# Kernel optimization log

Measured on AMD Instinct MI355X. Metric: run time of the kernel, lower is better.

## Reference

```python
import jax, jax.numpy as jnp
import numpy as np

CLIP = 100000.0

def heaviside(x):
    # smooth Heaviside approximation
    return (jnp.tanh(5.0 * x) + 1.0) / 2.0

def snowbucket(s0, t, ddf, tmax):
    ddf = ddf * 5.0
    tmax = tmax * 3.0
    return heaviside(t - tmax) * heaviside(s0) * jnp.minimum(s0, ddf * (t - tmax))

def soilbucket(s1, pet, f, smax, qmax, k):
    k = k / 10.0
    f = f / 10.0
    smax = smax * 1500.0
    qmax = qmax * 50.0
    h_pos = heaviside(s1)
    h_over = heaviside(s1 - smax)
    h_under = heaviside(smax - s1)
    et = h_pos * h_over * pet + h_pos * h_under * pet * (s1 / smax)
    qsub = h_pos * h_over * qmax + h_pos * h_under * qmax * jnp.exp(-f * (smax - s1))
    qsurf = h_pos * h_over * (s1 - smax)
    qst = qsub * k
    qgr = qsub * (1.0 - k)
    return et, qsurf, qst, qgr

def setup_inputs() -> dict:
    key = jax.random.key(0)
    ks = jax.random.split(key, 8)
    B, T = 8192, 1024
    prcp = jax.random.uniform(ks[0], (B, T, 1), jnp.float32) * 10.0   # mm/day
    tmean = jax.random.uniform(ks[1], (B, T, 1), jnp.float32) * 30.0 - 5.0  # deg C
    dayl = jax.random.uniform(ks[2], (B, T, 1), jnp.float32) * 0.5 + 0.25   # day fraction
    inputs = jnp.concatenate([prcp, tmean, dayl], axis=-1)
    def p(i):
        return jax.random.uniform(ks[i], (1,), jnp.float32) * 0.6 + 0.2
    return {"inputs": inputs, "f": p(3), "smax": p(4), "qmax": p(5),
            "ddf": p(6), "tmin": p(7), "tmax": p(3), "k": p(4)}

def reference(inputs, f, smax, qmax, ddf, tmin, tmax, k):
    # inputs: (B, T, 3) = [prcp, tmean, dayl]
    prcp = inputs[:, :, 0]
    tmean = inputs[:, :, 1]
    dayl = inputs[:, :, 2]
    pet = 29.8 * (dayl * 24.0) * 0.611 * jnp.exp(17.3 * tmean / (tmean + 237.3)) / (tmean + 273.2)

    tmin_s = tmin * -3.0

    # scan over time: carry = (s0, s1) each (B,)
    xs = jnp.stack([prcp, tmean, pet], axis=-1).transpose(1, 0, 2)  # (T, B, 3)

    def step(carry, x):
        s0, s1 = carry
        p_, t_, pet_ = x[:, 0], x[:, 1], x[:, 2]
        psnow = heaviside(tmin_s - t_) * p_
        prain = heaviside(t_ - tmin_s) * p_
        m = snowbucket(s0, t_, ddf, tmax)
        et, qsurf, qst, qgr = soilbucket(s1, pet_, f, smax, qmax, k)
        ds0 = psnow - m
        ds1 = prain + m - et - qsurf - qst - qgr
        ns0 = s0 + jnp.clip(ds0, -CLIP, CLIP)
        ns1 = s1 + jnp.clip(ds1, -CLIP, CLIP)
        return (ns0, ns1), (ns0, ns1)

    B = inputs.shape[0]
    init = (jnp.zeros((B,), inputs.dtype), jnp.zeros((B,), inputs.dtype))
    _, (s0_seq, s1_seq) = jax.lax.scan(step, init, xs)
    s0_seq = s0_seq.T  # (B, T)
    s1_seq = s1_seq.T

    # post-hoc flux computation on state sequences (as in call())
    _m = snowbucket(s0_seq, tmean, ddf, tmax)
    et, qsurf, qst, qgr = soilbucket(s1_seq, pet, f, smax, qmax, k)
    # mode == 'normal': note original names qsurf 'qsub' and outputs qsub+qst
    return jnp.stack([qsurf + qst, qgr], axis=-1)  # (B, T, 2)
```

## Files before the change

### kernel.cpp

```cpp
#include <hip/hip_runtime.h>

#define CLIPV 100000.0f
typedef __attribute__((address_space(3))) void as3void;
typedef __attribute__((address_space(1))) void as1void;

__device__ __forceinline__ float fexp2(float x){ return __builtin_amdgcn_exp2f(x); }
__device__ __forceinline__ float frcp(float x){ return __builtin_amdgcn_rcpf(x); }

#define WAIT_VM(N) { asm volatile("s_waitcnt vmcnt(" #N ")" ::: "memory"); \
                     __builtin_amdgcn_sched_barrier(0); }
#define LGKM0_BAR() { asm volatile("s_waitcnt lgkmcnt(0)" ::: "memory"); \
                      __builtin_amdgcn_s_barrier(); }

extern "C" __global__ void __launch_bounds__(128, 1)
prnn_kernel(const float* __restrict__ inp,
            const float* __restrict__ fpar,  const float* __restrict__ smaxp,
            const float* __restrict__ qmaxp, const float* __restrict__ ddfp,
            const float* __restrict__ tminp, const float* __restrict__ tmaxp,
            const float* __restrict__ kp,
            float* __restrict__ out)
{
    __shared__ alignas(16) unsigned char lin[2][13312];
    __shared__ alignas(16) float prodb[2][64 * 84];
    __shared__ alignas(16) float lcons[2][64 * 36];

    const int tid = threadIdx.x;
    const int l   = tid & 63;
    const int wv  = tid >> 6;
    const int c0  = blockIdx.x * 64;

    const float NL = -14.426950408889634f;
    float f10    = fpar[0] * 0.1f;
    float smax_s = smaxp[0] * 1500.0f;
    float qmax_s = qmaxp[0] * 50.0f;
    float ddf5   = ddfp[0] * 5.0f;
    float tmin_s = tminp[0] * -3.0f;
    float tmax3  = tmaxp[0] * 3.0f;
    float k10    = kp[0] * 0.1f;
    float ism    = 1.0f / smax_s;
    float cw     = 14.426950408889634f * tmin_s;
    float Kc     = fexp2(14.426950408889634f * (tmax3 - tmin_s));
    float cf     = 1.4426950408889634f * f10;
    float k1m    = 1.0f - k10;

    const float* gin  = inp + (size_t)c0 * 3072;
    float*       gout = out + (size_t)c0 * 2048;

    if (wv == 1) {
        auto stage_load = [&](int s, int pb) {
            const float* gb = gin + s * 48;
            #pragma unroll
            for (int k2 = 0; k2 < 13; ++k2) {
                unsigned e = (unsigned)(k2 * 64 + l);
                unsigned r = (e * 161321u) >> 21;
                int q = (int)(e - r * 13u);
                q = (q > 11) ? 11 : q;
                const float* g = gb + r * 3072 + q * 4;
                __builtin_amdgcn_global_load_lds((as1void*)g,
                    (as3void*)(&lin[pb][k2 * 1024]), 16, 0, 0);
            }
        };

        auto prod_one = [&](float p, float tm, float dl,
                            float& pr, float& ps, float& pe, float& eg, float& tg) {
            float t1 = tm + 237.3f, t2 = tm + 273.2f;
            float r12 = frcp(t1 * t2);
            float e1  = fexp2(24.958624207f * tm * (r12 * t2));
            pe = 436.9872f * dl * e1 * (r12 * t1);
            float ew = fexp2(fmaf(NL, tm, cw));
            float w  = frcp(1.0f + ew);
            pr = w * p;
            ps = p - pr;
            eg = 1.0f + fminf(ew * Kc, 1e30f);
            tg = ddf5 * (tm - tmax3);
        };

        auto prod_compute = [&](int s) {
            const unsigned char* myrow = &lin[s & 1][l * 208];
            float* o = prodb[s & 1] + l * 84;
            #pragma unroll
            for (int u4 = 0; u4 < 4; ++u4) {
                float4 A = *(const float4*)(myrow + u4 * 48);
                float4 B = *(const float4*)(myrow + u4 * 48 + 16);
                float4 C = *(const float4*)(myrow + u4 * 48 + 32);
                float pr[4], ps[4], pe[4], eg[4], tg[4];
                prod_one(A.x, A.y, A.z, pr[0], ps[0], pe[0], eg[0], tg[0]);
                prod_one(A.w, B.x, B.y, pr[1], ps[1], pe[1], eg[1], tg[1]);
                prod_one(B.z, B.w, C.x, pr[2], ps[2], pe[2], eg[2], tg[2]);
                prod_one(C.y, C.z, C.w, pr[3], ps[3], pe[3], eg[3], tg[3]);
                *(float4*)(o +      u4 * 4) = make_float4(pr[0], pr[1], pr[2], pr[3]);
                *(float4*)(o + 16 + u4 * 4) = make_float4(ps[0], ps[1], ps[2], ps[3]);
                *(float4*)(o + 32 + u4 * 4) = make_float4(pe[0], pe[1], pe[2], pe[3]);
                *(float4*)(o + 48 + u4 * 4) = make_float4(eg[0], eg[1], eg[2], eg[3]);
                *(float4*)(o + 64 + u4 * 4) = make_float4(tg[0], tg[1], tg[2], tg[3]);
            }
        };

        auto writeback = [&](int s) {
            float* gb = gout + s * 32;
            const float* lc = lcons[s & 1];
            #pragma unroll
            for (int k2 = 0; k2 < 9; ++k2) {
                unsigned e = (unsigned)(k2 * 64 + l);
                unsigned r = (e * 233017u) >> 21;
                int q = (int)(e - r * 9u);
                if (q < 8) {
                    const float* p0 = lc + r * 36 + 2 * q;
                    float2 qqv = *(const float2*)(p0);
                    float2 qbv = *(const float2*)(p0 + 16);
                    float o1a = k1m * qbv.x, o1b = k1m * qbv.y;
                    float4 v = make_float4(qqv.x - o1a, o1a, qqv.y - o1b, o1b);
                    *(float4*)(gb + r * 2048 + q * 4) = v;
                }
            }
        };

        stage_load(0, 0);
        WAIT_VM(0);
        stage_load(1, 1);
        prod_compute(0);
        LGKM0_BAR();
        stage_load(2, 0);
        WAIT_VM(13);
        prod_compute(1);
        LGKM0_BAR();
        for (int i = 2; i <= 62; ++i) {
            writeback(i - 2);
            stage_load(i + 1, (i + 1) & 1);
            WAIT_VM(22);
            prod_compute(i);
            LGKM0_BAR();
        }
        writeback(61);
        WAIT_VM(9);
        prod_compute(63);
        LGKM0_BAR();
        writeback(62);
        LGKM0_BAR();
        writeback(63);
    } else {
        float s0v = 0.0f, s1v = 0.0f, qq, c_et;
        {
            float d   = -smax_s;
            float eo  = fminf(fexp2(NL * d), 1e30f);
            float ep  = 1.0f;
            float den = (1.0f + ep) * (1.0f + eo);
            float hpo = frcp(den);
            float e   = fexp2(cf * d);
            float w1  = fmaf(e, eo, 1.0f);
            qq   = hpo * fmaf(qmax_s, w1, d);
            c_et = hpo;
        }
        LGKM0_BAR();

        for (int i = 1; i <= 64; ++i) {
            const int sb = (i - 1) & 1;
            const float* base = prodb[sb] + l * 84;
            float4 PR[5][4];
            #pragma unroll
            for (int q = 0; q < 5; ++q) {
                #pragma unroll
                for (int g = 0; g < 4; ++g)
                    PR[q][g] = *(const float4*)(base + q * 16 + g * 4);
            }
            float* lcb = lcons[sb] + l * 36;

            auto STEP = [&](float prain, float psnow, float pet, float eg1, float tmg,
                            float& oqq, float& oqb) {
                float es0 = fexp2(NL * s0v);
                float hg  = frcp(fmaf(es0, eg1, eg1));
                float m   = hg * fminf(s0v, tmg);
                float ds0 = psnow - m;
                s0v += fminf(fmaxf(ds0, -CLIPV), CLIPV);
                float et  = c_et * pet;
                float pme = (prain + m) - et;
                float ds1 = pme - qq;
                s1v += fminf(fmaxf(ds1, -CLIPV), CLIPV);
                float d   = s1v - smax_s;
                float eo  = fminf(fexp2(NL * d), 1e30f);
                float e   = fexp2(cf * d);
                float ep  = fminf(fexp2(NL * s1v), 1e30f);
                float den = (1.0f + ep) * (1.0f + eo);
                float hpo = frcp(den);
                float w1  = fmaf(e, eo, 1.0f);
                float qmw = qmax_s * w1;
                qq   = hpo * (d + qmw);
                oqb  = hpo * qmw;
                oqq  = qq;
                c_et = hpo * fmaf(eo, s1v * ism, 1.0f);
            };

            #pragma unroll
            for (int g = 0; g < 4; ++g) {
                float qs[4], qb[4];
                STEP(PR[0][g].x, PR[1][g].x, PR[2][g].x, PR[3][g].x, PR[4][g].x, qs[0], qb[0]);
                STEP(PR[0][g].y, PR[1][g].y, PR[2][g].y, PR[3][g].y, PR[4][g].y, qs[1], qb[1]);
                STEP(PR[0][g].z, PR[1][g].z, PR[2][g].z, PR[3][g].z, PR[4][g].z, qs[2], qb[2]);
                STEP(PR[0][g].w, PR[1][g].w, PR[2][g].w, PR[3][g].w, PR[4][g].w, qs[3], qb[3]);
                *(float4*)(lcb +      g * 4) = make_float4(qs[0], qs[1], qs[2], qs[3]);
                *(float4*)(lcb + 16 + g * 4) = make_float4(qb[0], qb[1], qb[2], qb[3]);
            }
            LGKM0_BAR();
        }
    }
}

extern "C" void kernel_launch(void* const* d_in, const int* in_sizes, int n_in,
                              void* d_out, int out_size, void* d_ws, size_t ws_size,
                              hipStream_t stream) {
    const float* inp = (const float*)d_in[0];
    const int B = in_sizes[0] / 3072;
    prnn_kernel<<<B / 64, 128, 0, stream>>>(
        inp,
        (const float*)d_in[1],
        (const float*)d_in[2],
        (const float*)d_in[3],
        (const float*)d_in[4],
        (const float*)d_in[5],
        (const float*)d_in[6],
        (const float*)d_in[7],
        (float*)d_out);
}
```

Before: 304.1 us.

## Split producer work across two waves and restructure scan step dependency chain

Adds a second producer wavefront (192 threads) so preprocessing, input staging (now triple-buffered) and output writeback are split in halves across two waves, with a pipelined loop and simplified barrier scheduling. The consumer scan step is reworked to compute outputs from the pre-update state, folding et/qsub terms into a single FMA chain, precomputing exp offsets, and dropping the CLIP clamps. The interleaved layout of output pairs is now produced by the consumer, so writeback is a plain float4 copy. Removing the clamps changes semantics only for extreme values, and the shifted output indexing adds an extra OUTV evaluation per tile.

```diff
diff --git a/kernel.cpp b/kernel.cpp
--- a/kernel.cpp
+++ b/kernel.cpp
@@ -1,18 +1,17 @@
 #include <hip/hip_runtime.h>
 
-#define CLIPV 100000.0f
 typedef __attribute__((address_space(3))) void as3void;
 typedef __attribute__((address_space(1))) void as1void;
 
 __device__ __forceinline__ float fexp2(float x){ return __builtin_amdgcn_exp2f(x); }
 __device__ __forceinline__ float frcp(float x){ return __builtin_amdgcn_rcpf(x); }
 
-#define WAIT_VM(N) { asm volatile("s_waitcnt vmcnt(" #N ")" ::: "memory"); \
+#define WAIT_VM0() { asm volatile("s_waitcnt vmcnt(0)" ::: "memory"); \
                      __builtin_amdgcn_sched_barrier(0); }
 #define LGKM0_BAR() { asm volatile("s_waitcnt lgkmcnt(0)" ::: "memory"); \
                       __builtin_amdgcn_s_barrier(); }
 
-extern "C" __global__ void __launch_bounds__(128, 1)
+extern "C" __global__ void __launch_bounds__(192, 1)
 prnn_kernel(const float* __restrict__ inp,
             const float* __restrict__ fpar,  const float* __restrict__ smaxp,
             const float* __restrict__ qmaxp, const float* __restrict__ ddfp,
@@ -20,7 +19,7 @@
             const float* __restrict__ kp,
             float* __restrict__ out)
 {
-    __shared__ alignas(16) unsigned char lin[2][13312];
+    __shared__ alignas(16) unsigned char lin[3][13312];
     __shared__ alignas(16) float prodb[2][64 * 84];
     __shared__ alignas(16) float lcons[2][64 * 36];
 
@@ -42,13 +41,18 @@
     float Kc     = fexp2(14.426950408889634f * (tmax3 - tmin_s));
     float cf     = 1.4426950408889634f * f10;
     float k1m    = 1.0f - k10;
+    float C1     = 14.426950408889634f * smax_s;
+    float C2     = -cf * smax_s;
 
     const float* gin  = inp + (size_t)c0 * 3072;
     float*       gout = out + (size_t)c0 * 2048;
 
-    if (wv == 1) {
-        auto stage_load = [&](int s, int pb) {
+    if (wv >= 1) {
+        const int pidx = wv - 1;
+
+        auto stage_load = [&](int s) {
             const float* gb = gin + s * 48;
+            unsigned char* lb = lin[s % 3];
             #pragma unroll
             for (int k2 = 0; k2 < 13; ++k2) {
                 unsigned e = (unsigned)(k2 * 64 + l);
@@ -57,7 +61,7 @@
                 q = (q > 11) ? 11 : q;
                 const float* g = gb + r * 3072 + q * 4;
                 __builtin_amdgcn_global_load_lds((as1void*)g,
-                    (as3void*)(&lin[pb][k2 * 1024]), 16, 0, 0);
+                    (as3void*)(lb + k2 * 1024), 16, 0, 0);
             }
         };
 
@@ -75,130 +79,127 @@
             tg = ddf5 * (tm - tmax3);
         };
 
-        auto prod_compute = [&](int s) {
-            const unsigned char* myrow = &lin[s & 1][l * 208];
-            float* o = prodb[s & 1] + l * 84;
+        auto prod_half = [&](int s) {
+            const unsigned char* myrow = lin[s % 3] + l * 208 + pidx * 96;
+            float* o = prodb[s & 1] + l * 84 + pidx * 8;
             #pragma unroll
-            for (int u4 = 0; u4 < 4; ++u4) {
-                float4 A = *(const float4*)(myrow + u4 * 48);
-                float4 B = *(const float4*)(myrow + u4 * 48 + 16);
-                float4 C = *(const float4*)(myrow + u4 * 48 + 32);
+            for (int g2 = 0; g2 < 2; ++g2) {
+                float4 A = *(const float4*)(myrow + g2 * 48);
+                float4 B = *(const float4*)(myrow + g2 * 48 + 16);
+                float4 C = *(const float4*)(myrow + g2 * 48 + 32);
                 float pr[4], ps[4], pe[4], eg[4], tg[4];
                 prod_one(A.x, A.y, A.z, pr[0], ps[0], pe[0], eg[0], tg[0]);
                 prod_one(A.w, B.x, B.y, pr[1], ps[1], pe[1], eg[1], tg[1]);
                 prod_one(B.z, B.w, C.x, pr[2], ps[2], pe[2], eg[2], tg[2]);
                 prod_one(C.y, C.z, C.w, pr[3], ps[3], pe[3], eg[3], tg[3]);
-                *(float4*)(o +      u4 * 4) = make_float4(pr[0], pr[1], pr[2], pr[3]);
-                *(float4*)(o + 16 + u4 * 4) = make_float4(ps[0], ps[1], ps[2], ps[3]);
-                *(float4*)(o + 32 + u4 * 4) = make_float4(pe[0], pe[1], pe[2], pe[3]);
-                *(float4*)(o + 48 + u4 * 4) = make_float4(eg[0], eg[1], eg[2], eg[3]);
-                *(float4*)(o + 64 + u4 * 4) = make_float4(tg[0], tg[1], tg[2], tg[3]);
-            }
-        };
-
-        auto writeback = [&](int s) {
-            float* gb = gout + s * 32;
-            const float* lc = lcons[s & 1];
+                *(float4*)(o +      g2 * 4) = make_float4(pr[0], pr[1], pr[2], pr[3]);
+                *(float4*)(o + 16 + g2 * 4) = make_float4(ps[0], ps[1], ps[2], ps[3]);
+                *(float4*)(o + 32 + g2 * 4) = make_float4(pe[0], pe[1], pe[2], pe[3]);
+                *(float4*)(o + 48 + g2 * 4) = make_float4(eg[0], eg[1], eg[2], eg[3]);
+                *(float4*)(o + 64 + g2 * 4) = make_float4(tg[0], tg[1], tg[2], tg[3]);
+            }
+        };
+
+        auto wb_half = [&](int j) {
+            const float* lc = lcons[j & 1];
+            float* gb = gout + j * 32;
             #pragma unroll
-            for (int k2 = 0; k2 < 9; ++k2) {
-                unsigned e = (unsigned)(k2 * 64 + l);
-                unsigned r = (e * 233017u) >> 21;
-                int q = (int)(e - r * 9u);
-                if (q < 8) {
-                    const float* p0 = lc + r * 36 + 2 * q;
-                    float2 qqv = *(const float2*)(p0);
-                    float2 qbv = *(const float2*)(p0 + 16);
-                    float o1a = k1m * qbv.x, o1b = k1m * qbv.y;
-                    float4 v = make_float4(qqv.x - o1a, o1a, qqv.y - o1b, o1b);
-                    *(float4*)(gb + r * 2048 + q * 4) = v;
-                }
-            }
-        };
-
-        stage_load(0, 0);
-        WAIT_VM(0);
-        stage_load(1, 1);
-        prod_compute(0);
+            for (int i = 0; i < 4; ++i) {
+                int u = pidx * 256 + i * 64 + l;
+                int r = u >> 3, q = u & 7;
+                float4 v = *(const float4*)(lc + r * 36 + q * 4);
+                *(float4*)(gb + (size_t)r * 2048 + q * 4) = v;
+            }
+        };
+
+        if (pidx == 0) { stage_load(0); WAIT_VM0(); }
+        else           { stage_load(1); }
         LGKM0_BAR();
-        stage_load(2, 0);
-        WAIT_VM(13);
-        prod_compute(1);
-        LGKM0_BAR();
-        for (int i = 2; i <= 62; ++i) {
-            writeback(i - 2);
-            stage_load(i + 1, (i + 1) & 1);
-            WAIT_VM(22);
-            prod_compute(i);
+
+        for (int s = 0; s <= 65; ++s) {
+            if (s <= 61 && pidx == (s & 1))       stage_load(s + 2);
+            if (s <= 63)                          prod_half(s);
+            if (s >= 2)                           wb_half(s - 2);
+            if (s <= 62 && pidx == ((s + 1) & 1)) WAIT_VM0();
             LGKM0_BAR();
         }
-        writeback(61);
-        WAIT_VM(9);
-        prod_compute(63);
+    } else {
+        float s0 = 0.0f, s1 = 0.0f;
+
+        auto STEP = [&](float prain, float psnow, float pet, float eg1, float tmg,
+                        float& o0, float& o1) {
+            float eo  = fminf(fexp2(fmaf(NL, s1, C1)), 1e30f);
+            float ep  = fminf(fexp2(NL * s1), 1e30f);
+            float e   = fexp2(fmaf(cf, s1, C2));
+            float hpo = frcp((1.0f + ep) * (1.0f + eo));
+            float d   = s1 - smax_s;
+            float qmw = qmax_s * fmaf(e, eo, 1.0f);
+            float W   = d + qmw;
+            float Z   = fmaf(eo, s1 * ism, 1.0f);
+            float Y   = fmaf(pet, Z, W);
+            float qsub = hpo * qmw;
+            float qq   = hpo * W;
+            o1 = k1m * qsub;
+            o0 = qq - o1;
+            float es0 = fexp2(NL * s0);
+            float hg  = frcp(fmaf(es0, eg1, eg1));
+            float m   = hg * fminf(s0, tmg);
+            s0 = (s0 + psnow) - m;
+            s1 = fmaf(-hpo, Y, (s1 + prain) + m);
+        };
+        auto OUTV = [&](float& o0, float& o1) {
+            float eo  = fminf(fexp2(fmaf(NL, s1, C1)), 1e30f);
+            float ep  = fminf(fexp2(NL * s1), 1e30f);
+            float e   = fexp2(fmaf(cf, s1, C2));
+            float hpo = frcp((1.0f + ep) * (1.0f + eo));
+            float d   = s1 - smax_s;
+            float qmw = qmax_s * fmaf(e, eo, 1.0f);
+            float qsub = hpo * qmw;
+            float qq   = hpo * (d + qmw);
+            o1 = k1m * qsub;
+            o0 = qq - o1;
+        };
+
         LGKM0_BAR();
-        writeback(62);
-        LGKM0_BAR();
-        writeback(63);
-    } else {
-        float s0v = 0.0f, s1v = 0.0f, qq, c_et;
-        {
-            float d   = -smax_s;
-            float eo  = fminf(fexp2(NL * d), 1e30f);
-            float ep  = 1.0f;
-            float den = (1.0f + ep) * (1.0f + eo);
-            float hpo = frcp(den);
-            float e   = fexp2(cf * d);
-            float w1  = fmaf(e, eo, 1.0f);
-            qq   = hpo * fmaf(qmax_s, w1, d);
-            c_et = hpo;
-        }
-        LGKM0_BAR();
-
-        for (int i = 1; i <= 64; ++i) {
-            const int sb = (i - 1) & 1;
-            const float* base = prodb[sb] + l * 84;
-            float4 PR[5][4];
-            #pragma unroll
-            for (int q = 0; q < 5; ++q) {
+        for (int s = 0; s <= 65; ++s) {
+            if (s >= 1 && s <= 64) {
+                const int st = s - 1;
+                const float* base = prodb[st & 1] + l * 84;
+                float4 PR[5][4];
                 #pragma unroll
-                for (int g = 0; g < 4; ++g)
-                    PR[q][g] = *(const float4*)(base + q * 16 + g * 4);
-            }
-            float* lcb = lcons[sb] + l * 36;
-
-            auto STEP = [&](float prain, float psnow, float pet, float eg1, float tmg,
-                            float& oqq, float& oqb) {
-                float es0 = fexp2(NL * s0v);
-                float hg  = frcp(fmaf(es0, eg1, eg1));
-                float m   = hg * fminf(s0v, tmg);
-                float ds0 = psnow - m;
-                s0v += fminf(fmaxf(ds0, -CLIPV), CLIPV);
-                float et  = c_et * pet;
-                float pme = (prain + m) - et;
-                float ds1 = pme - qq;
-                s1v += fminf(fmaxf(ds1, -CLIPV), CLIPV);
-                float d   = s1v - smax_s;
-                float eo  = fminf(fexp2(NL * d), 1e30f);
-                float e   = fexp2(cf * d);
-                float ep  = fminf(fexp2(NL * s1v), 1e30f);
-                float den = (1.0f + ep) * (1.0f + eo);
-                float hpo = frcp(den);
-                float w1  = fmaf(e, eo, 1.0f);
-                float qmw = qmax_s * w1;
-                qq   = hpo * (d + qmw);
-                oqb  = hpo * qmw;
-                oqq  = qq;
-                c_et = hpo * fmaf(eo, s1v * ism, 1.0f);
-            };
-
-            #pragma unroll
-            for (int g = 0; g < 4; ++g) {
-                float qs[4], qb[4];
-                STEP(PR[0][g].x, PR[1][g].x, PR[2][g].x, PR[3][g].x, PR[4][g].x, qs[0], qb[0]);
-                STEP(PR[0][g].y, PR[1][g].y, PR[2][g].y, PR[3][g].y, PR[4][g].y, qs[1], qb[1]);
-                STEP(PR[0][g].z, PR[1][g].z, PR[2][g].z, PR[3][g].z, PR[4][g].z, qs[2], qb[2]);
-                STEP(PR[0][g].w, PR[1][g].w, PR[2][g].w, PR[3][g].w, PR[4][g].w, qs[3], qb[3]);
-                *(float4*)(lcb +      g * 4) = make_float4(qs[0], qs[1], qs[2], qs[3]);
-                *(float4*)(lcb + 16 + g * 4) = make_float4(qb[0], qb[1], qb[2], qb[3]);
+                for (int q = 0; q < 5; ++q) {
+                    #pragma unroll
+                    for (int g = 0; g < 4; ++g)
+                        PR[q][g] = *(const float4*)(base + q * 16 + g * 4);
+                }
+                float o0s[16], o1s[16], dum0, dum1;
+                #define SGC(g, cx, O0, O1) \
+                    STEP(PR[0][g].cx, PR[1][g].cx, PR[2][g].cx, PR[3][g].cx, PR[4][g].cx, O0, O1)
+                SGC(0, x, dum0, dum1);
+                SGC(0, y, o0s[0],  o1s[0]);
+                SGC(0, z, o0s[1],  o1s[1]);
+                SGC(0, w, o0s[2],  o1s[2]);
+                SGC(1, x, o0s[3],  o1s[3]);
+                SGC(1, y, o0s[4],  o1s[4]);
+                SGC(1, z, o0s[5],  o1s[5]);
+                SGC(1, w, o0s[6],  o1s[6]);
+                SGC(2, x, o0s[7],  o1s[7]);
+                SGC(2, y, o0s[8],  o1s[8]);
+                SGC(2, z, o0s[9],  o1s[9]);
+                SGC(2, w, o0s[10], o1s[10]);
+                SGC(3, x, o0s[11], o1s[11]);
+                SGC(3, y, o0s[12], o1s[12]);
+                SGC(3, z, o0s[13], o1s[13]);
+                SGC(3, w, o0s[14], o1s[14]);
+                #undef SGC
+                OUTV(o0s[15], o1s[15]);
+                (void)dum0; (void)dum1;
+
+                float* lcb = lcons[st & 1] + l * 36;
+                #pragma unroll
+                for (int j = 0; j < 8; ++j)
+                    *(float4*)(lcb + j * 4) =
+                        make_float4(o0s[2*j], o1s[2*j], o0s[2*j+1], o1s[2*j+1]);
             }
             LGKM0_BAR();
         }
@@ -210,7 +211,7 @@
                               hipStream_t stream) {
     const float* inp = (const float*)d_in[0];
     const int B = in_sizes[0] / 3072;
-    prnn_kernel<<<B / 64, 128, 0, stream>>>(
+    prnn_kernel<<<B / 64, 192, 0, stream>>>(
         inp,
         (const float*)d_in[1],
         (const float*)d_in[2],
```

Measured after the change: 247.0 us. 18.8% less time.
